# Kernel optimization log

Hardware: AMD Instinct MI355X
Metric: run time of the kernel (lower is better)

## Reference

```python
import jax, jax.numpy as jnp
import numpy as np

N_NODES = 100000
N_EDGES = 1600000
N_REL = 8
IN_CH = 64
HIDDEN = 64
OUT_CH = 32


def setup_inputs() -> dict:
    key = jax.random.key(0)
    ks = jax.random.split(key, 10)
    s_in = 1.0 / np.sqrt(IN_CH)
    s_h = 1.0 / np.sqrt(HIDDEN)
    return {
        "x": jax.random.normal(ks[0], (N_NODES, IN_CH), dtype=jnp.float32),
        "edge_index": jax.random.randint(ks[1], (2, N_EDGES), 0, N_NODES, dtype=jnp.int64),
        "edge_type": jax.random.randint(ks[2], (N_EDGES,), 0, N_REL, dtype=jnp.int64),
        "W0": jax.random.normal(ks[3], (N_REL, IN_CH, HIDDEN), dtype=jnp.float32) * s_in,
        "Q0": jax.random.normal(ks[4], (HIDDEN, 1), dtype=jnp.float32) * s_h,
        "K0": jax.random.normal(ks[5], (HIDDEN, 1), dtype=jnp.float32) * s_h,
        "b0": jnp.zeros((HIDDEN,), dtype=jnp.float32),
        "W1": jax.random.normal(ks[6], (N_REL, HIDDEN, OUT_CH), dtype=jnp.float32) * s_h,
        "Q1": jax.random.normal(ks[7], (OUT_CH, 1), dtype=jnp.float32) * (1.0 / np.sqrt(OUT_CH)),
        "K1": jax.random.normal(ks[8], (OUT_CH, 1), dtype=jnp.float32) * (1.0 / np.sqrt(OUT_CH)),
        "b1": jnp.zeros((OUT_CH,), dtype=jnp.float32),
    }


def rgat_conv(x, src, dst, et, W, Q, K, b, n_nodes):
    # relation-typed transform of all nodes: [R, N, out]
    xw = jnp.einsum("ni,rio->rno", x, W)
    # per-node, per-relation attention logits (heads=1, dim=1)
    q = jnp.einsum("rno,od->rnd", xw, Q)[..., 0]  # [R, N]
    k = jnp.einsum("rno,od->rnd", xw, K)[..., 0]  # [R, N]
    # additive self-attention, leaky_relu slope 0.2 (PyG RGATConv default)
    alpha = jax.nn.leaky_relu(q[et, dst] + k[et, src], negative_slope=0.2)  # [E]
    # across-relation segment softmax over incoming edges of each dst node
    amax = jax.ops.segment_max(alpha, dst, num_segments=n_nodes)
    a = jnp.exp(alpha - amax[dst])
    denom = jax.ops.segment_sum(a, dst, num_segments=n_nodes)
    a = a / (denom[dst] + 1e-16)
    # weighted scatter-add aggregation of transformed source features
    msg = a[:, None] * xw[et, src]  # [E, out]
    return jax.ops.segment_sum(msg, dst, num_segments=n_nodes) + b


def reference(x, edge_index, edge_type, W0, Q0, K0, b0, W1, Q1, K1, b1):
    src, dst = edge_index[0], edge_index[1]
    n = x.shape[0]
    h = rgat_conv(x, src, dst, edge_type, W0, Q0, K0, b0, n)
    h = jax.nn.relu(h)  # dropout p=0.0 -> identity
    out = rgat_conv(h, src, dst, edge_type, W1, Q1, K1, b1, n)
    return out
```

## Files before the change

### kernel.cpp

```cpp
#include <hip/hip_runtime.h>
#include <hip/hip_bf16.h>
#include <math.h>


#define CSR_CHUNK 8192

__global__ void k_bhist(const int* __restrict__ dst, int* __restrict__ bcount,
                        int E, int NB) {
    __shared__ int h[512];
    int t = threadIdx.x;
    for (int i = t; i < NB; i += 256) h[i] = 0;
    __syncthreads();
    int e0 = blockIdx.x * CSR_CHUNK;
    int e1 = min(e0 + CSR_CHUNK, E);
    for (int i = e0 + t; i < e1; i += 256) atomicAdd(&h[dst[i] >> 8], 1);
    __syncthreads();
    for (int i = t; i < NB; i += 256) {
        int c = h[i];
        if (c) atomicAdd(&bcount[i], c);
    }
}

__global__ void k_bscan(const int* __restrict__ bcount, int* __restrict__ bstart,
                        int* __restrict__ gcur, int* __restrict__ rowptr,
                        int NB, int N, int E) {
    __shared__ int s[512];
    int t = threadIdx.x;
    int v = (t < NB) ? bcount[t] : 0;
    s[t] = v;
    __syncthreads();
    for (int off = 1; off < 512; off <<= 1) {
        int a = (t >= off) ? s[t - off] : 0;
        __syncthreads();
        s[t] += a;
        __syncthreads();
    }
    int excl = s[t] - v;
    if (t < NB) {
        bstart[t] = excl;
        gcur[t] = excl;
    }
    if (t == 0) {
        bstart[NB] = E;
        rowptr[N] = E;
    }
}

__global__ void k_bscatter(const int* __restrict__ src, const int* __restrict__ dst,
                           const int* __restrict__ et, int* __restrict__ gcur,
                           unsigned* __restrict__ ebuf, int E, int NB) {
    __shared__ int h[512];
    __shared__ int basearr[512];
    int t = threadIdx.x;
    for (int i = t; i < NB; i += 256) h[i] = 0;
    __syncthreads();
    int e0 = blockIdx.x * CSR_CHUNK;
    int e1 = min(e0 + CSR_CHUNK, E);
    for (int i = e0 + t; i < e1; i += 256) atomicAdd(&h[dst[i] >> 8], 1);
    __syncthreads();
    for (int i = t; i < NB; i += 256) {
        int c = h[i];
        basearr[i] = c ? atomicAdd(&gcur[i], c) : 0;
        h[i] = 0;
    }
    __syncthreads();
    for (int i = e0 + t; i < e1; i += 256) {
        int d = dst[i];
        int b = d >> 8;
        int off = atomicAdd(&h[b], 1);
        ebuf[basearr[b] + off] =
            ((unsigned)(d & 255) << 20) | ((unsigned)et[i] << 17) | (unsigned)src[i];
    }
}

__global__ void k_bsort(const unsigned* __restrict__ ebuf, const int* __restrict__ bstart,
                        int* __restrict__ rowptr, int* __restrict__ csr, int N) {
    __shared__ int lh[2048];
    __shared__ int ls[2048];
    __shared__ int ss[256];
    int b = blockIdx.x, t = threadIdx.x;
    int e0 = bstart[b], e1 = bstart[b + 1];
    for (int i = t; i < 2048; i += 256) lh[i] = 0;
    __syncthreads();
    for (int i = e0 + t; i < e1; i += 256) {
        unsigned u = ebuf[i];
        atomicAdd(&lh[(int)(((u >> 20) & 255) * 8 + ((u >> 17) & 7))], 1);
    }
    __syncthreads();
    int loc[8];
    int s = 0;
#pragma unroll
    for (int j = 0; j < 8; j++) {
        loc[j] = s;
        s += lh[t * 8 + j];
    }
    ss[t] = s;
    __syncthreads();
    for (int off = 1; off < 256; off <<= 1) {
        int a = (t >= off) ? ss[t - off] : 0;
        __syncthreads();
        ss[t] += a;
        __syncthreads();
    }
    int excl = ss[t] - s;
#pragma unroll
    for (int j = 0; j < 8; j++) ls[t * 8 + j] = excl + loc[j];
    int node = b * 256 + t;
    if (node < N) rowptr[node] = e0 + excl;
    __syncthreads();
    for (int i = t; i < 2048; i += 256) lh[i] = 0;
    __syncthreads();
    for (int i = e0 + t; i < e1; i += 256) {
        unsigned u = ebuf[i];
        int key = (int)(((u >> 20) & 255) * 8 + ((u >> 17) & 7));
        int off = atomicAdd(&lh[key], 1);
        csr[e0 + ls[key] + off] = (int)u;
    }
}


__global__ void k_wt2(const float* __restrict__ W, __hip_bfloat16* __restrict__ hi,
                      __hip_bfloat16* __restrict__ lo, int OUT, int total) {
    int t = blockIdx.x * blockDim.x + threadIdx.x;
    if (t < total) {
        int per = 64 * OUT;
        int r = t / per;
        int rem = t % per;
        int i = rem / OUT;
        int o = rem % OUT;
        float v = W[t];
        __hip_bfloat16 h = __float2bfloat16(v);
        __hip_bfloat16 l = __float2bfloat16(v - __bfloat162float(h));
        size_t idx = (size_t)o * 512 + i * 8 + r;
        hi[idx] = h;
        lo[idx] = l;
    }
}

__global__ void k_wqk(const float* W, const float* Qv, const float* Kv,
                      float* wq, float* wk, int OUT) {
    int t = blockIdx.x * blockDim.x + threadIdx.x;
    if (t < 8 * 64) {
        int r = t >> 6, i = t & 63;
        const float* wrow = W + ((size_t)r * 64 + i) * OUT;
        float a = 0.f, b = 0.f;
        for (int o = 0; o < OUT; o++) {
            float w = wrow[o];
            a += w * Qv[o];
            b += w * Kv[o];
        }
        wq[t] = a;
        wk[t] = b;
    }
}

__global__ __launch_bounds__(256) void k_qk2(
        const float* __restrict__ xin, const float* __restrict__ wq,
        const float* __restrict__ wk, float* __restrict__ qn,
        float* __restrict__ kn, unsigned short* __restrict__ xbb, int N) {
    __shared__ float xt[64][65];
    __shared__ float swq[8 * 65], swk[8 * 65];
    int t = threadIdx.x;
    int nb0 = blockIdx.x * 64;
    for (int i = t; i < 512; i += 256) {
        int r = i >> 6, c = i & 63;
        swq[r * 65 + c] = wq[i];
        swk[r * 65 + c] = wk[i];
    }
    for (int i = t; i < 1024; i += 256) {
        int ns = i >> 4;
        int c4 = i & 15;
        int n = nb0 + ns;
        float4 v = {0.f, 0.f, 0.f, 0.f};
        if (n < N) v = ((const float4*)xin)[(size_t)n * 16 + c4];
        xt[ns][c4 * 4 + 0] = v.x;
        xt[ns][c4 * 4 + 1] = v.y;
        xt[ns][c4 * 4 + 2] = v.z;
        xt[ns][c4 * 4 + 3] = v.w;
        if (n < N) {
            __hip_bfloat16 b0 = __float2bfloat16(v.x);
            __hip_bfloat16 b1 = __float2bfloat16(v.y);
            __hip_bfloat16 b2 = __float2bfloat16(v.z);
            __hip_bfloat16 b3 = __float2bfloat16(v.w);
            ushort4 o;
            o.x = *(unsigned short*)&b0;
            o.y = *(unsigned short*)&b1;
            o.z = *(unsigned short*)&b2;
            o.w = *(unsigned short*)&b3;
            *(ushort4*)(xbb + (size_t)n * 64 + c4 * 4) = o;
        }
    }
    __syncthreads();
#pragma unroll
    for (int g = t; g < 512; g += 256) {
        int ns = g >> 3, r = g & 7;
        int n = nb0 + ns;
        if (n < N) {
            float qa = 0.f, ka = 0.f;
#pragma unroll
            for (int i = 0; i < 64; i++) {
                float xv = xt[ns][i];
                qa += xv * swq[r * 65 + i];
                ka += xv * swk[r * 65 + i];
            }
            qn[(size_t)n * 8 + r] = qa;
            kn[(size_t)n * 8 + r] = ka;
        }
    }
}

#define ZSTR 520
#define EMAX 512

#define FLUSH8()                          \
    do {                                  \
        switch (currel) {                 \
            case 0: a0 += racc; break;    \
            case 1: a1 += racc; break;    \
            case 2: a2 += racc; break;    \
            case 3: a3 += racc; break;    \
            case 4: a4 += racc; break;    \
            case 5: a5 += racc; break;    \
            case 6: a6 += racc; break;    \
            case 7: a7 += racc; break;    \
        }                                 \
    } while (0)

template <int OUT, bool RELU>
__global__ __launch_bounds__(256) void k_fused(
        const int* __restrict__ rowptr, const int* __restrict__ csr,
        const float* __restrict__ qn, const float* __restrict__ kn,
        const unsigned short* __restrict__ xb,
        const __hip_bfloat16* __restrict__ wthi,
        const __hip_bfloat16* __restrict__ wtlo,
        const float* __restrict__ bias, float* __restrict__ xout, int N) {
    using v8s = __attribute__((ext_vector_type(8))) short;
    using v4f = __attribute__((ext_vector_type(4))) float;
    __shared__ unsigned short zt[16 * ZSTR];
    __shared__ uint2 s_rec[EMAX];
    __shared__ float s_q[128];
    int t = threadIdx.x;
    int wv = t >> 6;
    int lane = t & 63;
    int nb0 = blockIdx.x * 16;

    if (t < 128) {
        int nd = nb0 + (t >> 3);
        s_q[t] = (nd < N) ? qn[(size_t)nd * 8 + (t & 7)] : 0.f;
    }
    int e0 = rowptr[nb0];
    int eend = rowptr[min(nb0 + 16, N)];
    int esz = eend - e0;
    __syncthreads();

    if (esz <= EMAX) {
        for (int i = t; i < esz; i += 256) {
            int pk = csr[e0 + i];
            int nl = (pk >> 20) & 15;
            int rel = (pk >> 17) & 7;
            int src = pk & 0x1FFFF;
            float v = s_q[nl * 8 + rel] + kn[(size_t)src * 8 + rel];
            v = (v >= 0.f) ? v : 0.2f * v;
            float tv = __expf(v);
            s_rec[i] = uint2{__float_as_uint(tv), (unsigned)pk};
        }
        __syncthreads();

#pragma unroll 1
        for (int q = 0; q < 4; q++) {
            int nl = wv * 4 + q;
            int wid = nb0 + nl;
            uint4 pack = {0u, 0u, 0u, 0u};
            if (wid < N) {
                int r0 = rowptr[wid] - e0;
                int r1 = rowptr[wid + 1] - e0;
                float a0 = 0.f, a1 = 0.f, a2 = 0.f, a3 = 0.f;
                float a4 = 0.f, a5 = 0.f, a6 = 0.f, a7 = 0.f;
                float racc = 0.f, denom = 0.f;
                int currel = 0;
#pragma unroll 1
                for (int j = r0; j < r1; j += 16) {
                    float tvv[16];
                    int pkk[16];
#pragma unroll
                    for (int u = 0; u < 16; u++) {
                        int ii = j + u;
                        bool ok = ii < r1;
                        ii = ok ? ii : (r1 - 1);
                        uint2 rc = s_rec[ii];
                        tvv[u] = __uint_as_float(
                            __builtin_amdgcn_readfirstlane((int)(ok ? rc.x : 0u)));
                        pkk[u] = __builtin_amdgcn_readfirstlane((int)rc.y);
                    }
                    unsigned short xu[16];
#pragma unroll
                    for (int u = 0; u < 16; u++)
                        xu[u] = xb[(size_t)(pkk[u] & 0x1FFFF) * 64 + lane];
#pragma unroll
                    for (int u = 0; u < 16; u++) {
                        int rl = (pkk[u] >> 17) & 7;
                        if (rl != currel) {
                            FLUSH8();
                            currel = rl;
                            racc = 0.f;
                        }
                        racc += tvv[u] * __uint_as_float(((unsigned)xu[u]) << 16);
                        denom += tvv[u];
                    }
                }
                FLUSH8();
                float inv = 1.f / (denom + 1e-16f);
                float av[8] = {a0, a1, a2, a3, a4, a5, a6, a7};
                unsigned short us[8];
#pragma unroll
                for (int r = 0; r < 8; r++) {
                    __hip_bfloat16 b = __float2bfloat16(av[r] * inv);
                    us[r] = *(unsigned short*)&b;
                }
                pack.x = (unsigned)us[0] | ((unsigned)us[1] << 16);
                pack.y = (unsigned)us[2] | ((unsigned)us[3] << 16);
                pack.z = (unsigned)us[4] | ((unsigned)us[5] << 16);
                pack.w = (unsigned)us[6] | ((unsigned)us[7] << 16);
            }
            *(uint4*)&zt[nl * ZSTR + lane * 8] = pack;
        }
    } else {
        for (int q = 0; q < 4; q++) {
            int nl = wv * 4 + q;
            int wid = nb0 + nl;
            uint4 pack = {0u, 0u, 0u, 0u};
            if (wid < N) {
                int r0 = rowptr[wid], r1 = rowptr[wid + 1];
                float qv = (lane < 8) ? qn[wid * 8 + lane] : 0.f;
                float denom = 0.f;
                float a0 = 0.f, a1 = 0.f, a2 = 0.f, a3 = 0.f;
                float a4 = 0.f, a5 = 0.f, a6 = 0.f, a7 = 0.f;
                int currel = 0;
                float racc = 0.f;

                for (int base = r0; base < r1; base += 64) {
                    int s = base + lane;
                    int pk = (s < r1) ? csr[s] : 0;
                    int src = pk & 0x1FFFF;
                    int rel = (pk >> 17) & 7;
                    float qq = __shfl(qv, rel, 64);
                    float tv = 0.f;
                    if (s < r1) {
                        float v = qq + kn[src * 8 + rel];
                        v = (v >= 0.f) ? v : 0.2f * v;
                        tv = __expf(v);
                    }
                    float ts = tv;
#pragma unroll
                    for (int off = 32; off > 0; off >>= 1) ts += __shfl_xor(ts, off, 64);
                    denom += ts;

                    int cnt = min(64, r1 - base);
                    int tvi = (int)__float_as_uint(tv);
                    for (int j = 0; j < cnt; j += 16) {
                        unsigned p[16];
                        float tf[16];
#pragma unroll
                        for (int u = 0; u < 16; u++) {
                            p[u] = (unsigned)__builtin_amdgcn_readlane(pk, j + u);
                            tf[u] = __uint_as_float(
                                (unsigned)__builtin_amdgcn_readlane(tvi, j + u));
                        }
                        unsigned xg[16];
#pragma unroll
                        for (int u = 0; u < 16; u++)
                            xg[u] = (unsigned)xb[(size_t)(p[u] & 0x1FFFF) * 64 + lane];
#pragma unroll
                        for (int u = 0; u < 16; u++) {
                            int rl = (int)((p[u] >> 17) & 7);
                            if (rl != currel) {
                                FLUSH8();
                                currel = rl;
                                racc = 0.f;
                            }
                            racc += tf[u] * __uint_as_float(xg[u] << 16);
                        }
                    }
                }
                FLUSH8();
                float inv = 1.f / (denom + 1e-16f);
                float av[8] = {a0, a1, a2, a3, a4, a5, a6, a7};
                unsigned short us[8];
#pragma unroll
                for (int r = 0; r < 8; r++) {
                    __hip_bfloat16 b = __float2bfloat16(av[r] * inv);
                    us[r] = *(unsigned short*)&b;
                }
                pack.x = (unsigned)us[0] | ((unsigned)us[1] << 16);
                pack.y = (unsigned)us[2] | ((unsigned)us[3] << 16);
                pack.z = (unsigned)us[4] | ((unsigned)us[5] << 16);
                pack.w = (unsigned)us[6] | ((unsigned)us[7] << 16);
            }
            *(uint4*)&zt[nl * ZSTR + lane * 8] = pack;
        }
    }
    __syncthreads();

    int quad = lane >> 4;
    int l15 = lane & 15;
    int nt = wv;
    if (nt * 16 < OUT) {
        const short* wh = (const short*)wthi;
        const short* wl = (const short*)wtlo;
        v4f acc = {0.f, 0.f, 0.f, 0.f};
#pragma unroll
        for (int k0 = 0; k0 < 512; k0 += 32) {
            int koff = k0 + quad * 8;
            v8s A = *(const v8s*)&zt[l15 * ZSTR + koff];
            v8s bh = *(const v8s*)(wh + (size_t)(nt * 16 + l15) * 512 + koff);
            v8s bl = *(const v8s*)(wl + (size_t)(nt * 16 + l15) * 512 + koff);
            acc = __builtin_amdgcn_mfma_f32_16x16x32_bf16(A, bh, acc, 0, 0, 0);
            acc = __builtin_amdgcn_mfma_f32_16x16x32_bf16(A, bl, acc, 0, 0, 0);
        }
        float bcol = bias[nt * 16 + l15];
#pragma unroll
        for (int g = 0; g < 4; g++) {
            int row = nb0 + quad * 4 + g;
            if (row < N) {
                float o = acc[g] + bcol;
                if (RELU) o = fmaxf(o, 0.f);
                xout[(size_t)row * OUT + nt * 16 + l15] = o;
            }
        }
    }
}


extern "C" void kernel_launch(void* const* d_in, const int* in_sizes, int n_in,
                              void* d_out, int out_size, void* d_ws, size_t ws_size,
                              hipStream_t stream) {
    const float* x   = (const float*)d_in[0];
    const int*   ei  = (const int*)d_in[1];
    const int*   et  = (const int*)d_in[2];
    const float* W0  = (const float*)d_in[3];
    const float* Q0  = (const float*)d_in[4];
    const float* K0  = (const float*)d_in[5];
    const float* b0  = (const float*)d_in[6];
    const float* W1  = (const float*)d_in[7];
    const float* Q1  = (const float*)d_in[8];
    const float* K1  = (const float*)d_in[9];
    const float* b1  = (const float*)d_in[10];
    float* out = (float*)d_out;

    const int N = in_sizes[0] / 64;
    const int E = in_sizes[2];
    const int* src = ei;
    const int* dst = ei + E;
    const int NB = (N + 255) >> 8;

    char* p = (char*)d_ws;
    auto alloc = [&](size_t bytes) -> void* {
        void* r = (void*)p;
        p += ((bytes + 255) / 256) * 256;
        return r;
    };
    int* rowptr   = (int*)alloc((size_t)(N + 1) * 4);
    int* bcount   = (int*)alloc(513 * 4);
    int* bstart   = (int*)alloc(513 * 4);
    int* gcur     = (int*)alloc(513 * 4);
    unsigned* ebuf = (unsigned*)alloc((size_t)E * 4);
    int* csr      = (int*)alloc((size_t)E * 4);
    float* wq     = (float*)alloc(8 * 64 * 4);
    float* wk     = (float*)alloc(8 * 64 * 4);
    float* qn     = (float*)alloc((size_t)N * 8 * 4);
    float* kn     = (float*)alloc((size_t)N * 8 * 4);
    __hip_bfloat16* wthi = (__hip_bfloat16*)alloc((size_t)64 * 512 * 2);
    __hip_bfloat16* wtlo = (__hip_bfloat16*)alloc((size_t)64 * 512 * 2);
    float* h      = (float*)alloc((size_t)N * 64 * 4);
    unsigned short* xbb = (unsigned short*)alloc((size_t)N * 64 * 2);

    int nchunks = (E + CSR_CHUNK - 1) / CSR_CHUNK;
    hipMemsetAsync(bcount, 0, (size_t)NB * 4, stream);
    k_bhist<<<nchunks, 256, 0, stream>>>(dst, bcount, E, NB);
    k_bscan<<<1, 512, 0, stream>>>(bcount, bstart, gcur, rowptr, NB, N, E);
    k_bscatter<<<nchunks, 256, 0, stream>>>(src, dst, et, gcur, ebuf, E, NB);
    k_bsort<<<NB, 256, 0, stream>>>(ebuf, bstart, rowptr, csr, N);

    int nfb = (N + 15) / 16;
    int nqkb = (N + 63) / 64;

    k_wqk<<<2, 256, 0, stream>>>(W0, Q0, K0, wq, wk, 64);
    k_qk2<<<nqkb, 256, 0, stream>>>(x, wq, wk, qn, kn, xbb, N);
    k_wt2<<<(8 * 64 * 64 + 255) / 256, 256, 0, stream>>>(W0, wthi, wtlo, 64, 8 * 64 * 64);
    k_fused<64, true><<<nfb, 256, 0, stream>>>(rowptr, csr, qn, kn, xbb,
                                               wthi, wtlo, b0, h, N);

    k_wqk<<<2, 256, 0, stream>>>(W1, Q1, K1, wq, wk, 32);
    k_qk2<<<nqkb, 256, 0, stream>>>(h, wq, wk, qn, kn, xbb, N);
    k_wt2<<<(8 * 64 * 32 + 255) / 256, 256, 0, stream>>>(W1, wthi, wtlo, 32, 8 * 64 * 32);
    k_fused<32, false><<<nfb, 256, 0, stream>>>(rowptr, csr, qn, kn, xbb,
                                                wthi, wtlo, b1, out, N);
}
```

Baseline: 448.1 us.

## Partition edges by source-node slice for cache-local split aggregation

Result: slower. 1.405 ms (+213.5%).

```diff
diff --git a/kernel.cpp b/kernel.cpp
--- a/kernel.cpp
+++ b/kernel.cpp
@@ -1,5 +1,6 @@
 #include <hip/hip_runtime.h>
 #include <hip/hip_bf16.h>
+#include <hip/hip_fp16.h>
 #include <math.h>
 
 
@@ -22,7 +23,7 @@
 }
 
 __global__ void k_bscan(const int* __restrict__ bcount, int* __restrict__ bstart,
-                        int* __restrict__ gcur, int* __restrict__ rowptr,
+                        int* __restrict__ gcur, int* __restrict__ rp3,
                         int NB, int N, int E) {
     __shared__ int s[512];
     int t = threadIdx.x;
@@ -40,10 +41,8 @@
         bstart[t] = excl;
         gcur[t] = excl;
     }
-    if (t == 0) {
-        bstart[NB] = E;
-        rowptr[N] = E;
-    }
+    if (t == 0) bstart[NB] = E;
+    if (t < 8) rp3[(size_t)N * 8 + t] = E;
 }
 
 __global__ void k_bscatter(const int* __restrict__ src, const int* __restrict__ dst,
@@ -74,25 +73,27 @@
 }
 
 __global__ void k_bsort(const unsigned* __restrict__ ebuf, const int* __restrict__ bstart,
-                        int* __restrict__ rowptr, int* __restrict__ csr, int N) {
-    __shared__ int lh[2048];
-    __shared__ int ls[2048];
+                        int* __restrict__ rp3, int* __restrict__ csr, int N, int NS) {
+    __shared__ int lh[16384];
     __shared__ int ss[256];
     int b = blockIdx.x, t = threadIdx.x;
     int e0 = bstart[b], e1 = bstart[b + 1];
-    for (int i = t; i < 2048; i += 256) lh[i] = 0;
+    for (int i = t; i < 16384; i += 256) lh[i] = 0;
     __syncthreads();
     for (int i = e0 + t; i < e1; i += 256) {
         unsigned u = ebuf[i];
-        atomicAdd(&lh[(int)(((u >> 20) & 255) * 8 + ((u >> 17) & 7))], 1);
-    }
-    __syncthreads();
-    int loc[8];
+        int dl = (u >> 20) & 255;
+        int rel = (u >> 17) & 7;
+        int w = min((int)(u & 0x1FFFF) / NS, 7);
+        atomicAdd(&lh[dl * 64 + w * 8 + rel], 1);
+    }
+    __syncthreads();
     int s = 0;
-#pragma unroll
-    for (int j = 0; j < 8; j++) {
-        loc[j] = s;
-        s += lh[t * 8 + j];
+#pragma unroll 1
+    for (int k = 0; k < 64; k++) {
+        int c = lh[t * 64 + k];
+        lh[t * 64 + k] = s;
+        s += c;
     }
     ss[t] = s;
     __syncthreads();
@@ -103,18 +104,23 @@
         __syncthreads();
     }
     int excl = ss[t] - s;
-#pragma unroll
-    for (int j = 0; j < 8; j++) ls[t * 8 + j] = excl + loc[j];
+#pragma unroll 1
+    for (int k = 0; k < 64; k++) lh[t * 64 + k] += excl;
+    __syncthreads();
     int node = b * 256 + t;
-    if (node < N) rowptr[node] = e0 + excl;
-    __syncthreads();
-    for (int i = t; i < 2048; i += 256) lh[i] = 0;
+    if (node < N) {
+#pragma unroll
+        for (int p2 = 0; p2 < 8; p2++)
+            rp3[(size_t)node * 8 + p2] = e0 + lh[t * 64 + p2 * 8];
+    }
     __syncthreads();
     for (int i = e0 + t; i < e1; i += 256) {
         unsigned u = ebuf[i];
-        int key = (int)(((u >> 20) & 255) * 8 + ((u >> 17) & 7));
-        int off = atomicAdd(&lh[key], 1);
-        csr[e0 + ls[key] + off] = (int)u;
+        int dl = (u >> 20) & 255;
+        int rel = (u >> 17) & 7;
+        int w = min((int)(u & 0x1FFFF) / NS, 7);
+        int pos = e0 + atomicAdd(&lh[dl * 64 + w * 8 + rel], 1);
+        csr[pos] = (int)u;
     }
 }
 
@@ -226,9 +232,215 @@
         }                                 \
     } while (0)
 
+template <int OUT>
+__global__ __launch_bounds__(256) void k_agg(
+        const int* __restrict__ rp3, const int* __restrict__ csr,
+        const float* __restrict__ qn, const float* __restrict__ kn,
+        const unsigned short* __restrict__ xb,
+        const __hip_bfloat16* __restrict__ wthi,
+        const __hip_bfloat16* __restrict__ wtlo,
+        __half* __restrict__ pout, float* __restrict__ pden, int N) {
+    using v8s = __attribute__((ext_vector_type(8))) short;
+    using v4f = __attribute__((ext_vector_type(4))) float;
+    __shared__ unsigned short zt[16 * ZSTR];
+    int t = threadIdx.x;
+    int wvu = __builtin_amdgcn_readfirstlane(t >> 6);
+    int lane = t & 63;
+    int b = blockIdx.x;
+    int slice = b & 7;
+    int nb0 = (b >> 3) * 16;
+
+#pragma unroll 1
+    for (int q = 0; q < 4; q++) {
+        int nl = wvu * 4 + q;
+        int wid = nb0 + nl;
+        uint4 pack = {0u, 0u, 0u, 0u};
+        if (wid < N) {
+            int r0 = rp3[(size_t)wid * 8 + slice];
+            int r1 = (slice < 7) ? rp3[(size_t)wid * 8 + slice + 1]
+                                 : rp3[(size_t)(wid + 1) * 8];
+            int qvec = 0;
+            if (lane < 8) qvec = ((const int*)qn)[wid * 8 + lane];
+            float a0 = 0.f, a1 = 0.f, a2 = 0.f, a3 = 0.f;
+            float a4 = 0.f, a5 = 0.f, a6 = 0.f, a7 = 0.f;
+            float racc = 0.f, denom = 0.f;
+            int currel = 0;
+#pragma unroll 1
+            for (int j = r0; j < r1; j += 4) {
+                int pk[4];
+                float kv[4];
+                unsigned short xu[4];
+#pragma unroll
+                for (int u = 0; u < 4; u++) {
+                    int ii = (j + u < r1) ? (j + u) : (r1 - 1);
+                    pk[u] = csr[ii];
+                }
+#pragma unroll
+                for (int u = 0; u < 4; u++)
+                    kv[u] = kn[(size_t)(pk[u] & 0x1FFFF) * 8 + ((pk[u] >> 17) & 7)];
+#pragma unroll
+                for (int u = 0; u < 4; u++)
+                    xu[u] = xb[(size_t)(pk[u] & 0x1FFFF) * 64 + lane];
+#pragma unroll
+                for (int u = 0; u < 4; u++) {
+                    int rl = (pk[u] >> 17) & 7;
+                    float qv = __uint_as_float(__builtin_amdgcn_readlane(qvec, rl));
+                    float v = qv + kv[u];
+                    v = fmaxf(v, 0.2f * v);
+                    float tv = __expf(v);
+                    if (j + u >= r1) tv = 0.f;
+                    if (rl != currel) {
+                        FLUSH8();
+                        currel = rl;
+                        racc = 0.f;
+                    }
+                    racc += tv * __uint_as_float(((unsigned)xu[u]) << 16);
+                    denom += tv;
+                }
+            }
+            FLUSH8();
+            float inv = (denom > 0.f) ? 1.f / denom : 0.f;
+            float av[8] = {a0, a1, a2, a3, a4, a5, a6, a7};
+            unsigned short us[8];
+#pragma unroll
+            for (int r = 0; r < 8; r++) {
+                __hip_bfloat16 bb = __float2bfloat16(av[r] * inv);
+                us[r] = *(unsigned short*)&bb;
+            }
+            pack.x = (unsigned)us[0] | ((unsigned)us[1] << 16);
+            pack.y = (unsigned)us[2] | ((unsigned)us[3] << 16);
+            pack.z = (unsigned)us[4] | ((unsigned)us[5] << 16);
+            pack.w = (unsigned)us[6] | ((unsigned)us[7] << 16);
+            if (lane == 0) pden[(size_t)slice * N + wid] = denom;
+        }
+        *(uint4*)&zt[nl * ZSTR + lane * 8] = pack;
+    }
+    __syncthreads();
+
+    int quad = lane >> 4;
+    int l15 = lane & 15;
+    int nt = wvu;
+    if (nt * 16 < OUT) {
+        const short* wh = (const short*)wthi;
+        const short* wl = (const short*)wtlo;
+        v4f acc = {0.f, 0.f, 0.f, 0.f};
+#pragma unroll
+        for (int k0 = 0; k0 < 512; k0 += 32) {
+            int koff = k0 + quad * 8;
+            v8s A = *(const v8s*)&zt[l15 * ZSTR + koff];
+            v8s bh = *(const v8s*)(wh + (size_t)(nt * 16 + l15) * 512 + koff);
+            v8s bl = *(const v8s*)(wl + (size_t)(nt * 16 + l15) * 512 + koff);
+            acc = __builtin_amdgcn_mfma_f32_16x16x32_bf16(A, bh, acc, 0, 0, 0);
+            acc = __builtin_amdgcn_mfma_f32_16x16x32_bf16(A, bl, acc, 0, 0, 0);
+        }
+#pragma unroll
+        for (int g = 0; g < 4; g++) {
+            int row = nb0 + quad * 4 + g;
+            if (row < N) {
+                __half hv = __float2half(acc[g]);
+                __builtin_nontemporal_store(
+                    *(short*)&hv,
+                    (short*)(pout + ((size_t)slice * N + row) * OUT + nt * 16 + l15));
+            }
+        }
+    }
+}
+
+template <int OUT, bool RELU, bool QK>
+__global__ __launch_bounds__(256) void k_fin(
+        const __half* __restrict__ pout, const float* __restrict__ pden,
+        const float* __restrict__ bias, const float* __restrict__ wq,
+        const float* __restrict__ wk, float* __restrict__ qn,
+        float* __restrict__ kn, unsigned short* __restrict__ xbb,
+        float* __restrict__ fout, int N) {
+    __shared__ float xt[64][65];
+    __shared__ float swq[8 * 65], swk[8 * 65];
+    __shared__ float spd[64][9];
+    int t = threadIdx.x;
+    int nb0 = blockIdx.x * 64;
+    if (QK) {
+        for (int i = t; i < 512; i += 256) {
+            int r = i >> 6, c = i & 63;
+            swq[r * 65 + c] = wq[i];
+            swk[r * 65 + c] = wk[i];
+        }
+    }
+    for (int i = t; i < 512; i += 256) {
+        int ns = i >> 3, s = i & 7;
+        int n = nb0 + ns;
+        spd[ns][s] = (n < N) ? pden[(size_t)s * N + n] : 0.f;
+    }
+    __syncthreads();
+    if (t < 64) {
+        float D = 0.f;
+#pragma unroll
+        for (int s = 0; s < 8; s++) D += spd[t][s];
+        spd[t][8] = 1.f / (D + 1e-16f);
+    }
+    __syncthreads();
+    constexpr int D4 = OUT / 4;
+    for (int i = t; i < 64 * D4; i += 256) {
+        int ns = i / D4, d4 = i % D4;
+        int n = nb0 + ns;
+        if (n < N) {
+            float v[4] = {0.f, 0.f, 0.f, 0.f};
+#pragma unroll
+            for (int s = 0; s < 8; s++) {
+                float w = spd[ns][s];
+                const __half* pr = pout + ((size_t)s * N + n) * OUT + d4 * 4;
+#pragma unroll
+                for (int k = 0; k < 4; k++) v[k] += w * __half2float(pr[k]);
+            }
+            float inv = spd[ns][8];
+#pragma unroll
+            for (int k = 0; k < 4; k++) {
+                float o = v[k] * inv + bias[d4 * 4 + k];
+                if (RELU) o = fmaxf(o, 0.f);
+                v[k] = o;
+            }
+            if (QK) {
+#pragma unroll
+                for (int k = 0; k < 4; k++) xt[ns][d4 * 4 + k] = v[k];
+                __hip_bfloat16 b0 = __float2bfloat16(v[0]);
+                __hip_bfloat16 b1 = __float2bfloat16(v[1]);
+                __hip_bfloat16 b2 = __float2bfloat16(v[2]);
+                __hip_bfloat16 b3 = __float2bfloat16(v[3]);
+                ushort4 o4;
+                o4.x = *(unsigned short*)&b0;
+                o4.y = *(unsigned short*)&b1;
+                o4.z = *(unsigned short*)&b2;
+                o4.w = *(unsigned short*)&b3;
+                *(ushort4*)(xbb + (size_t)n * 64 + d4 * 4) = o4;
+            } else {
+#pragma unroll
+                for (int k = 0; k < 4; k++)
+                    fout[(size_t)n * OUT + d4 * 4 + k] = v[k];
+            }
+        }
+    }
+    if (QK) {
+        __syncthreads();
+        for (int g = t; g < 512; g += 256) {
+            int ns = g >> 3, r = g & 7;
+            int n = nb0 + ns;
+            if (n < N) {
+                float qa = 0.f, ka = 0.f;
+#pragma unroll
+                for (int i2 = 0; i2 < 64; i2++) {
+                    float xv = xt[ns][i2];
+                    qa += xv * swq[r * 65 + i2];
+                    ka += xv * swk[r * 65 + i2];
+                }
+                qn[(size_t)n * 8 + r] = qa;
+                kn[(size_t)n * 8 + r] = ka;
+            }
+        }
+    }
+}
+
 template <int OUT, bool RELU>
 __global__ __launch_bounds__(256) void k_fused(
-        const int* __restrict__ rowptr, const int* __restrict__ csr,
+        const int* __restrict__ rp3, const int* __restrict__ csr,
         const float* __restrict__ qn, const float* __restrict__ kn,
         const unsigned short* __restrict__ xb,
         const __hip_bfloat16* __restrict__ wthi,
@@ -248,8 +460,8 @@
         int nd = nb0 + (t >> 3);
         s_q[t] = (nd < N) ? qn[(size_t)nd * 8 + (t & 7)] : 0.f;
     }
-    int e0 = rowptr[nb0];
-    int eend = rowptr[min(nb0 + 16, N)];
+    int e0 = rp3[(size_t)nb0 * 8];
+    int eend = rp3[(size_t)min(nb0 + 16, N) * 8];
     int esz = eend - e0;
     __syncthreads();
 
@@ -272,8 +484,8 @@
             int wid = nb0 + nl;
             uint4 pack = {0u, 0u, 0u, 0u};
             if (wid < N) {
-                int r0 = rowptr[wid] - e0;
-                int r1 = rowptr[wid + 1] - e0;
+                int r0 = rp3[(size_t)wid * 8] - e0;
+                int r1 = rp3[(size_t)(wid + 1) * 8] - e0;
                 float a0 = 0.f, a1 = 0.f, a2 = 0.f, a3 = 0.f;
                 float a4 = 0.f, a5 = 0.f, a6 = 0.f, a7 = 0.f;
                 float racc = 0.f, denom = 0.f;
@@ -314,8 +526,8 @@
                 unsigned short us[8];
 #pragma unroll
                 for (int r = 0; r < 8; r++) {
-                    __hip_bfloat16 b = __float2bfloat16(av[r] * inv);
-                    us[r] = *(unsigned short*)&b;
+                    __hip_bfloat16 bb = __float2bfloat16(av[r] * inv);
+                    us[r] = *(unsigned short*)&bb;
                 }
                 pack.x = (unsigned)us[0] | ((unsigned)us[1] << 16);
                 pack.y = (unsigned)us[2] | ((unsigned)us[3] << 16);
@@ -330,7 +542,7 @@
             int wid = nb0 + nl;
             uint4 pack = {0u, 0u, 0u, 0u};
             if (wid < N) {
-                int r0 = rowptr[wid], r1 = rowptr[wid + 1];
+                int r0 = rp3[(size_t)wid * 8], r1 = rp3[(size_t)(wid + 1) * 8];
                 float qv = (lane < 8) ? qn[wid * 8 + lane] : 0.f;
                 float denom = 0.f;
                 float a0 = 0.f, a1 = 0.f, a2 = 0.f, a3 = 0.f;
@@ -388,8 +600,8 @@
                 unsigned short us[8];
 #pragma unroll
                 for (int r = 0; r < 8; r++) {
-                    __hip_bfloat16 b = __float2bfloat16(av[r] * inv);
-                    us[r] = *(unsigned short*)&b;
+                    __hip_bfloat16 bb = __float2bfloat16(av[r] * inv);
+                    us[r] = *(unsigned short*)&bb;
                 }
                 pack.x = (unsigned)us[0] | ((unsigned)us[1] << 16);
                 pack.y = (unsigned)us[2] | ((unsigned)us[3] << 16);
@@ -452,6 +664,7 @@
     const int* src = ei;
     const int* dst = ei + E;
     const int NB = (N + 255) >> 8;
+    const int NS = (N + 7) / 8;
 
     char* p = (char*)d_ws;
     auto alloc = [&](size_t bytes) -> void* {
@@ -459,7 +672,7 @@
         p += ((bytes + 255) / 256) * 256;
         return r;
     };
-    int* rowptr   = (int*)alloc((size_t)(N + 1) * 4);
+    int* rp3      = (int*)alloc(((size_t)N + 1) * 8 * 4);
     int* bcount   = (int*)alloc(513 * 4);
     int* bstart   = (int*)alloc(513 * 4);
     int* gcur     = (int*)alloc(513 * 4);
@@ -471,15 +684,21 @@
     float* kn     = (float*)alloc((size_t)N * 8 * 4);
     __hip_bfloat16* wthi = (__hip_bfloat16*)alloc((size_t)64 * 512 * 2);
     __hip_bfloat16* wtlo = (__hip_bfloat16*)alloc((size_t)64 * 512 * 2);
-    float* h      = (float*)alloc((size_t)N * 64 * 4);
     unsigned short* xbb = (unsigned short*)alloc((size_t)N * 64 * 2);
+    char* psave = p;
+    __half* pout = (__half*)alloc((size_t)8 * N * 64 * 2);
+    float* pden  = (float*)alloc((size_t)8 * N * 4);
+    size_t need_new = (size_t)(p - (char*)d_ws);
+    p = psave;
+    float* h = (float*)alloc((size_t)N * 64 * 4);
+    bool newok = (need_new <= ws_size) && (NB <= 512);
 
     int nchunks = (E + CSR_CHUNK - 1) / CSR_CHUNK;
     hipMemsetAsync(bcount, 0, (size_t)NB * 4, stream);
     k_bhist<<<nchunks, 256, 0, stream>>>(dst, bcount, E, NB);
-    k_bscan<<<1, 512, 0, stream>>>(bcount, bstart, gcur, rowptr, NB, N, E);
+    k_bscan<<<1, 512, 0, stream>>>(bcount, bstart, gcur, rp3, NB, N, E);
     k_bscatter<<<nchunks, 256, 0, stream>>>(src, dst, et, gcur, ebuf, E, NB);
-    k_bsort<<<NB, 256, 0, stream>>>(ebuf, bstart, rowptr, csr, N);
+    k_bsort<<<NB, 256, 0, stream>>>(ebuf, bstart, rp3, csr, N, NS);
 
     int nfb = (N + 15) / 16;
     int nqkb = (N + 63) / 64;
@@ -487,12 +706,27 @@
     k_wqk<<<2, 256, 0, stream>>>(W0, Q0, K0, wq, wk, 64);
     k_qk2<<<nqkb, 256, 0, stream>>>(x, wq, wk, qn, kn, xbb, N);
     k_wt2<<<(8 * 64 * 64 + 255) / 256, 256, 0, stream>>>(W0, wthi, wtlo, 64, 8 * 64 * 64);
-    k_fused<64, true><<<nfb, 256, 0, stream>>>(rowptr, csr, qn, kn, xbb,
-                                               wthi, wtlo, b0, h, N);
-
-    k_wqk<<<2, 256, 0, stream>>>(W1, Q1, K1, wq, wk, 32);
-    k_qk2<<<nqkb, 256, 0, stream>>>(h, wq, wk, qn, kn, xbb, N);
-    k_wt2<<<(8 * 64 * 32 + 255) / 256, 256, 0, stream>>>(W1, wthi, wtlo, 32, 8 * 64 * 32);
-    k_fused<32, false><<<nfb, 256, 0, stream>>>(rowptr, csr, qn, kn, xbb,
-                                                wthi, wtlo, b1, out, N);
-}
+
+    if (newok) {
+        k_agg<64><<<nfb * 8, 256, 0, stream>>>(rp3, csr, qn, kn, xbb,
+                                               wthi, wtlo, pout, pden, N);
+        k_wqk<<<2, 256, 0, stream>>>(W1, Q1, K1, wq, wk, 32);
+        k_fin<64, true, true><<<nqkb, 256, 0, stream>>>(
+            pout, pden, b0, wq, wk, qn, kn, xbb, nullptr, N);
+        k_wt2<<<(8 * 64 * 32 + 255) / 256, 256, 0, stream>>>(W1, wthi, wtlo, 32,
+                                                             8 * 64 * 32);
+        k_agg<32><<<nfb * 8, 256, 0, stream>>>(rp3, csr, qn, kn, xbb,
+                                               wthi, wtlo, pout, pden, N);
+        k_fin<32, false, false><<<nqkb, 256, 0, stream>>>(
+            pout, pden, b1, nullptr, nullptr, nullptr, nullptr, nullptr, out, N);
+    } else {
+        k_fused<64, true><<<nfb, 256, 0, stream>>>(rp3, csr, qn, kn, xbb,
+                                                   wthi, wtlo, b0, h, N);
+        k_wqk<<<2, 256, 0, stream>>>(W1, Q1, K1, wq, wk, 32);
+        k_qk2<<<nqkb, 256, 0, stream>>>(h, wq, wk, qn, kn, xbb, N);
+        k_wt2<<<(8 * 64 * 32 + 255) / 256, 256, 0, stream>>>(W1, wthi, wtlo, 32,
+                                                             8 * 64 * 32);
+        k_fused<32, false><<<nfb, 256, 0, stream>>>(rp3, csr, qn, kn, xbb,
+                                                    wthi, wtlo, b1, out, N);
+    }
+}
```
